# Kernel tuning notes

Measured on AMD Instinct MI355X. Metric: run time of the kernel, lower is better.

Reference implementation:

```python
import jax, jax.numpy as jnp
import numpy as np

B, C, H, W, K = 32, 10, 256, 256, 500
EPS = 1e-7


def setup_inputs() -> dict:
    key = jax.random.key(0)
    k1, k2, k3 = jax.random.split(key, 3)
    pred_wh = jax.random.normal(k1, (B, C, H, W), dtype=jnp.float32)
    wh_target = jax.random.normal(k2, (B, K, C), dtype=jnp.float32)
    reg_mask = jnp.ones((B, K), dtype=jnp.float32)
    ind = jax.random.randint(k3, (B, K), 0, H * W, dtype=jnp.int32)
    return {"pred_wh": pred_wh, "wh_target": wh_target, "reg_mask": reg_mask, "ind": ind}


def _cal_box(p):
    # p: [8] = (tt, rr, bb, ll) point offsets -> 4 corners centered at (tt+bb)/2
    tt, rr, bb, ll = p[0:2], p[2:4], p[4:6], p[6:8]
    cen = (tt + bb) * 0.5
    return jnp.stack([tt + rr, bb + rr, bb + ll, tt + ll]) - cen  # [4,2] tr,br,bl,tl


def _sort_ccw(pts):
    c = pts.mean(axis=0)
    ang = jnp.arctan2(pts[:, 1] - c[1], pts[:, 0] - c[0])
    return pts[jnp.argsort(ang)]


def _shoelace(pts):
    x, y = pts[:, 0], pts[:, 1]
    return 0.5 * jnp.abs(jnp.sum(x * jnp.roll(y, -1) - jnp.roll(x, -1) * y))


def _convex_inter_area(A, Bp):
    # A, Bp: [4,2] CCW-ordered convex quads. Intersection area via
    # candidate points (verts-inside + edge-edge crossings) of the convex overlap.
    An, Bn = jnp.roll(A, -1, axis=0), jnp.roll(Bp, -1, axis=0)

    def inside(P, poly, polyn):  # all-edges left-of test for CCW poly
        ex, ey = (polyn - poly)[:, 0], (polyn - poly)[:, 1]
        px = P[:, None, 0] - poly[None, :, 0]
        py = P[:, None, 1] - poly[None, :, 1]
        return jnp.all(ex[None, :] * py - ey[None, :] * px >= -EPS, axis=1)

    mA = inside(A, Bp, Bn)
    mB = inside(Bp, A, An)

    a1, a2 = A[:, None, :], An[:, None, :]
    b1, b2 = Bp[None, :, :], Bn[None, :, :]
    d1, d2 = a2 - a1, b2 - b1
    den = d1[..., 0] * d2[..., 1] - d1[..., 1] * d2[..., 0]
    diff = b1 - a1
    safe = jnp.where(jnp.abs(den) > EPS, den, 1.0)
    t = (diff[..., 0] * d2[..., 1] - diff[..., 1] * d2[..., 0]) / safe
    u = (diff[..., 0] * d1[..., 1] - diff[..., 1] * d1[..., 0]) / safe
    mI = (jnp.abs(den) > EPS) & (t >= -EPS) & (t <= 1 + EPS) & (u >= -EPS) & (u <= 1 + EPS)
    pI = a1 + t[..., None] * d1  # [4,4,2]

    pts = jnp.concatenate([A, Bp, pI.reshape(16, 2)], axis=0)  # [24,2]
    valid = jnp.concatenate([mA, mB, mI.reshape(16)], axis=0)  # [24]
    first = pts[jnp.argmax(valid)]
    pts = jnp.where(valid[:, None], pts, first)  # dup invalids onto a hull vertex
    nv = jnp.maximum(valid.sum(), 1)
    c = jnp.sum(pts * valid[:, None], axis=0) / nv
    ang = jnp.arctan2(pts[:, 1] - c[1], pts[:, 0] - c[0])
    area = _shoelace(pts[jnp.argsort(ang)])
    return jnp.where(valid.any(), area, 0.0)


def _per_box(a, b):
    A = _sort_ccw(_cal_box(a))
    Bq = _sort_ccw(_cal_box(b))
    inter = _convex_inter_area(A, Bq)
    union = _shoelace(A) + _shoelace(Bq) - inter
    iou = jnp.where(union > 0, inter / jnp.where(union > 0, union, 1.0), 0.0)

    w = jnp.sqrt((a[2] - a[6]) ** 2 + (a[3] - a[7]) ** 2)
    h = jnp.sqrt((a[0] - a[4]) ** 2 + (a[1] - a[5]) ** 2)
    wt = jnp.sqrt((b[2] - b[6]) ** 2 + (b[3] - a[7]) ** 2)  # faithful: source uses a[7]
    ht = jnp.sqrt((b[0] - b[4]) ** 2 + (b[1] - b[5]) ** 2)
    th1 = (a[3] - a[7]) / (a[2] - a[6])
    tth1 = (b[3] - b[7]) / (b[2] - b[6])
    th = (a[1] - a[5]) / (a[0] - a[4])
    tth = (b[1] - b[5]) / (b[0] - b[4])
    n = jnp.minimum((jnp.arctan(th) - jnp.arctan(tth)) ** 2,
                    (jnp.arctan(th1) - jnp.arctan(tth1)) ** 2)
    c4 = 4.0 / (np.pi ** 2)
    v = c4 * (jnp.arctan(wt / ht) - jnp.arctan(w / h)) ** 2
    s = c4 * n
    alpha = (v + s) / (1.0 - iou + v + s)
    return alpha * (v + 0.7 * s)


def reference(pred_wh, wh_target, reg_mask, ind):
    b, c, h, w = pred_wh.shape
    feat = pred_wh.transpose(0, 2, 3, 1).reshape(b, h * w, c)
    pred = jnp.take_along_axis(feat, ind[:, :, None].astype(jnp.int32), axis=1)  # [B,K,C]
    pa = pred.reshape(-1, c)[:, :8]
    ga = wh_target.reshape(-1, c)[:, :8]
    losses = jax.vmap(_per_box)(pa, ga)  # [B*K]
    mflat = reg_mask.reshape(-1) > 0
    n = mflat.shape[0]
    last = jnp.max(jnp.where(mflat, jnp.arange(n), -1))
    # original loop overwrites `loss` each iter -> final value is the LAST masked box
    loss = jnp.where(mflat.any(), losses[jnp.maximum(last, 0)], 0.0)
    # everything feeding the loss is under torch.no_grad()/numpy -> detached
    return jax.lax.stop_gradient(loss)
```

## Files before the change

kernel.cpp:

```cpp
#include <hip/hip_runtime.h>
#include <math.h>

#define BB 32
#define CC 10
#define HH 256
#define WW 256
#define KK 500

constexpr double DEPS = 1e-7;

__device__ inline double dshfl(double v, int lane) { return __shfl(v, lane, 64); }

__device__ inline double shoelace4(const double* x, const double* y) {
    double s = x[0]*y[1] - x[1]*y[0];
    s += x[1]*y[2] - x[2]*y[1];
    s += x[2]*y[3] - x[3]*y[2];
    s += x[3]*y[0] - x[0]*y[3];
    return 0.5 * fabs(s);
}

__device__ void cal_box_sorted(const double p[8], double X[4], double Y[4]) {
    double cenx = (p[0] + p[4]) * 0.5;
    double ceny = (p[1] + p[5]) * 0.5;
    double px[4] = { p[0] + p[2] - cenx, p[4] + p[2] - cenx,
                     p[4] + p[6] - cenx, p[0] + p[6] - cenx };
    double py[4] = { p[1] + p[3] - ceny, p[5] + p[3] - ceny,
                     p[5] + p[7] - ceny, p[1] + p[7] - ceny };
    double cx = (px[0] + px[1] + px[2] + px[3]) * 0.25;
    double cy = (py[0] + py[1] + py[2] + py[3]) * 0.25;
    float ang[4];
    #pragma unroll
    for (int i = 0; i < 4; ++i)
        ang[i] = atan2f((float)(py[i] - cy), (float)(px[i] - cx));
    int idx[4] = {0, 1, 2, 3};
    #pragma unroll
    for (int i = 1; i < 4; ++i) {
        int key = idx[i]; float ka = ang[key]; int j = i - 1;
        while (j >= 0 && ang[idx[j]] > ka) { idx[j + 1] = idx[j]; --j; }
        idx[j + 1] = key;
    }
    #pragma unroll
    for (int i = 0; i < 4; ++i) { X[i] = px[idx[i]]; Y[i] = py[idx[i]]; }
}

__global__ __launch_bounds__(1024)
void IouLoss_26766236189166_kernel(const float* __restrict__ pred_wh,
                                   const float* __restrict__ wh_target,
                                   const float* __restrict__ reg_mask,
                                   const int* __restrict__ ind,
                                   float* __restrict__ out) {
    __shared__ int s_wave[16];
    __shared__ int s_last;
    const int tid = threadIdx.x;

    const float4* rm = (const float4*)reg_mask;
    const int N4 = (BB * KK) / 4;
    int last = -1;
    for (int chunk = 3; chunk >= 0; --chunk) {
        int lmax = -1;
        int i = chunk * 1024 + tid;
        if (i < N4) {
            float4 v = rm[i];
            if (v.x > 0.f) lmax = 4 * i;
            if (v.y > 0.f) lmax = 4 * i + 1;
            if (v.z > 0.f) lmax = 4 * i + 2;
            if (v.w > 0.f) lmax = 4 * i + 3;
        }
        #pragma unroll
        for (int off = 32; off > 0; off >>= 1)
            lmax = max(lmax, __shfl_down(lmax, off, 64));
        if ((tid & 63) == 0) s_wave[tid >> 6] = lmax;
        __syncthreads();
        if (tid == 0) {
            int m = -1;
            #pragma unroll
            for (int w = 0; w < 16; ++w) m = max(m, s_wave[w]);
            s_last = m;
        }
        __syncthreads();
        last = s_last;
        if (last >= 0) break;
    }

    if (tid >= 64) return;
    const int k = tid;

    float loss = 0.0f;
    if (last >= 0) {
        const int b   = last / KK;
        const int kk_ = last - b * KK;
        const int pix = ind[last];

        double a[8], g[8];
        const float* pw = pred_wh + (size_t)b * CC * (HH * WW) + pix;
        const float* gt = wh_target + ((size_t)b * KK + kk_) * CC;
        #pragma unroll
        for (int c = 0; c < 8; ++c) a[c] = (double)pw[(size_t)c * (HH * WW)];
        #pragma unroll
        for (int c = 0; c < 8; ++c) g[c] = (double)gt[c];

        double AX[4], AY[4], BX[4], BY[4];
        cal_box_sorted(a, AX, AY);
        cal_box_sorted(g, BX, BY);

        bool valid = false; double px = 0.0, py = 0.0;
        if (k < 4) {
            bool ok = true;
            #pragma unroll
            for (int j = 0; j < 4; ++j) {
                int jn = (j + 1) & 3;
                double ex = BX[jn] - BX[j], ey = BY[jn] - BY[j];
                double qx = AX[k] - BX[j], qy = AY[k] - BY[j];
                ok = ok && (ex * qy - ey * qx >= -DEPS);
            }
            valid = ok; px = AX[k]; py = AY[k];
        } else if (k < 8) {
            int i = k - 4;
            bool ok = true;
            #pragma unroll
            for (int j = 0; j < 4; ++j) {
                int jn = (j + 1) & 3;
                double ex = AX[jn] - AX[j], ey = AY[jn] - AY[j];
                double qx = BX[i] - AX[j], qy = BY[i] - AY[j];
                ok = ok && (ex * qy - ey * qx >= -DEPS);
            }
            valid = ok; px = BX[i]; py = BY[i];
        } else if (k < 24) {
            int i = (k - 8) >> 2, j = (k - 8) & 3;
            int in_ = (i + 1) & 3, jn = (j + 1) & 3;
            double a1x = AX[i], a1y = AY[i];
            double d1x = AX[in_] - a1x, d1y = AY[in_] - a1y;
            double b1x = BX[j], b1y = BY[j];
            double d2x = BX[jn] - b1x, d2y = BY[jn] - b1y;
            double den = d1x * d2y - d1y * d2x;
            double dx = b1x - a1x, dy = b1y - a1y;
            bool dok = fabs(den) > DEPS;
            double safe = dok ? den : 1.0;
            double t = (dx * d2y - dy * d2x) / safe;
            double u = (dx * d1y - dy * d1x) / safe;
            valid = dok && (t >= -DEPS) && (t <= 1.0 + DEPS)
                        && (u >= -DEPS) && (u <= 1.0 + DEPS);
            px = a1x + t * d1x;
            py = a1y + t * d1y;
        }

        unsigned long long mv = __ballot(valid);
        bool any = (mv != 0ull);
        int nv  = __popcll(mv);
        int nvd = nv < 1 ? 1 : nv;
        int fi  = any ? ((int)__ffsll(mv) - 1) : 0;
        double fx = dshfl(px, fi), fy = dshfl(py, fi);
        if (k < 24 && !valid) { px = fx; py = fy; }

        double cxs = valid ? px : 0.0, cys = valid ? py : 0.0;
        #pragma unroll
        for (int off = 32; off > 0; off >>= 1) {
            cxs += __shfl_xor(cxs, off, 64);
            cys += __shfl_xor(cys, off, 64);
        }
        double cx = cxs / (double)nvd, cy = cys / (double)nvd;

        float ang = (k < 24) ? atan2f((float)(py - cy), (float)(px - cx)) : INFINITY;
        int r = 0;
        #pragma unroll
        for (int j = 0; j < 24; ++j) {
            float aj = __shfl(ang, j, 64);
            r += (aj < ang) || (aj == ang && j < k);
        }
        if (k >= 24) r = k;

        int addr = r << 2;
        int xlo = __builtin_amdgcn_ds_permute(addr, __double2loint(px));
        int xhi = __builtin_amdgcn_ds_permute(addr, __double2hiint(px));
        int ylo = __builtin_amdgcn_ds_permute(addr, __double2loint(py));
        int yhi = __builtin_amdgcn_ds_permute(addr, __double2hiint(py));
        double sxp = __hiloint2double(xhi, xlo);
        double syp = __hiloint2double(yhi, ylo);

        int nxt = (k < 23) ? (k + 1) : ((k == 23) ? 0 : k);
        double nx = dshfl(sxp, nxt);
        double ny = dshfl(syp, nxt);
        double term = (k < 24) ? (sxp * ny - nx * syp) : 0.0;
        #pragma unroll
        for (int off = 32; off > 0; off >>= 1)
            term += __shfl_xor(term, off, 64);
        double inter = any ? 0.5 * fabs(term) : 0.0;

        double areaA = shoelace4(AX, AY);
        double areaB = shoelace4(BX, BY);
        double uni = areaA + areaB - inter;
        double iou = (uni > 0.0) ? (inter / uni) : 0.0;

        double w  = sqrt((a[2]-a[6])*(a[2]-a[6]) + (a[3]-a[7])*(a[3]-a[7]));
        double h  = sqrt((a[0]-a[4])*(a[0]-a[4]) + (a[1]-a[5])*(a[1]-a[5]));
        double wt = sqrt((g[2]-g[6])*(g[2]-g[6]) + (g[3]-a[7])*(g[3]-a[7]));
        double ht = sqrt((g[0]-g[4])*(g[0]-g[4]) + (g[1]-g[5])*(g[1]-g[5]));

        double num = (k==0) ? (a[1]-a[5]) : (k==1) ? (g[1]-g[5]) :
                     (k==2) ? (a[3]-a[7]) : (k==3) ? (g[3]-g[7]) :
                     (k==4) ? wt : w;
        double den = (k==0) ? (a[0]-a[4]) : (k==1) ? (g[0]-g[4]) :
                     (k==2) ? (a[2]-a[6]) : (k==3) ? (g[2]-g[6]) :
                     (k==4) ? ht : h;
        double at = atan(num / den);
        double t_th   = dshfl(at, 0);
        double t_tth  = dshfl(at, 1);
        double t_th1  = dshfl(at, 2);
        double t_tth1 = dshfl(at, 3);
        double t_awt  = dshfl(at, 4);
        double t_aw   = dshfl(at, 5);

        double d1v = t_th  - t_tth;
        double d2v = t_th1 - t_tth1;
        double nn = fmin(d1v * d1v, d2v * d2v);
        const double c4 = 4.0 / (M_PI * M_PI);
        double dvv = t_awt - t_aw;
        double v = c4 * dvv * dvv;
        double sv = c4 * nn;
        double alpha = (v + sv) / (1.0 - iou + v + sv);
        loss = (float)(alpha * (v + 0.7 * sv));
    }

    if (tid == 0) out[0] = loss;
}

extern "C" void kernel_launch(void* const* d_in, const int* in_sizes, int n_in,
                              void* d_out, int out_size, void* d_ws, size_t ws_size,
                              hipStream_t stream) {
    const float* pred_wh   = (const float*)d_in[0];
    const float* wh_target = (const float*)d_in[1];
    const float* reg_mask  = (const float*)d_in[2];
    const int*   ind       = (const int*)d_in[3];
    float* out = (float*)d_out;
    IouLoss_26766236189166_kernel<<<dim3(1), dim3(1024), 0, stream>>>(
        pred_wh, wh_target, reg_mask, ind, out);
}
```

Measured before the change: 13.31 us.

## Scan reg_mask backward with a single wave and fuse ind lookup

```diff
diff --git a/kernel.cpp b/kernel.cpp
--- a/kernel.cpp
+++ b/kernel.cpp
@@ -43,53 +43,47 @@
     for (int i = 0; i < 4; ++i) { X[i] = px[idx[i]]; Y[i] = py[idx[i]]; }
 }
 
-__global__ __launch_bounds__(1024)
+__global__ __launch_bounds__(64)
 void IouLoss_26766236189166_kernel(const float* __restrict__ pred_wh,
                                    const float* __restrict__ wh_target,
                                    const float* __restrict__ reg_mask,
                                    const int* __restrict__ ind,
                                    float* __restrict__ out) {
-    __shared__ int s_wave[16];
-    __shared__ int s_last;
-    const int tid = threadIdx.x;
-
+    const int k = threadIdx.x;
     const float4* rm = (const float4*)reg_mask;
+    const int4*   iv = (const int4*)ind;
     const int N4 = (BB * KK) / 4;
-    int last = -1;
-    for (int chunk = 3; chunk >= 0; --chunk) {
-        int lmax = -1;
-        int i = chunk * 1024 + tid;
-        if (i < N4) {
+
+    int last = -1, pix = 0;
+    for (int base = N4 - 64; base > -64; base -= 64) {
+        int i = base + k;
+        int lmax = -1, pcand = 0;
+        if (i >= 0) {
             float4 v = rm[i];
-            if (v.x > 0.f) lmax = 4 * i;
-            if (v.y > 0.f) lmax = 4 * i + 1;
-            if (v.z > 0.f) lmax = 4 * i + 2;
-            if (v.w > 0.f) lmax = 4 * i + 3;
-        }
-        #pragma unroll
-        for (int off = 32; off > 0; off >>= 1)
-            lmax = max(lmax, __shfl_down(lmax, off, 64));
-        if ((tid & 63) == 0) s_wave[tid >> 6] = lmax;
-        __syncthreads();
-        if (tid == 0) {
-            int m = -1;
-            #pragma unroll
-            for (int w = 0; w < 16; ++w) m = max(m, s_wave[w]);
-            s_last = m;
-        }
-        __syncthreads();
-        last = s_last;
-        if (last >= 0) break;
+            int4  iq = iv[i];
+            if (v.x > 0.f) { lmax = 4*i;     pcand = iq.x; }
+            if (v.y > 0.f) { lmax = 4*i + 1; pcand = iq.y; }
+            if (v.z > 0.f) { lmax = 4*i + 2; pcand = iq.z; }
+            if (v.w > 0.f) { lmax = 4*i + 3; pcand = iq.w; }
+        }
+        unsigned long long packed =
+            ((unsigned long long)(unsigned)(lmax + 1) << 32) | (unsigned)pcand;
+        #pragma unroll
+        for (int off = 32; off > 0; off >>= 1) {
+            unsigned long long o = __shfl_xor(packed, off, 64);
+            packed = (o > packed) ? o : packed;
+        }
+        if ((packed >> 32) != 0ull) {
+            last = (int)(packed >> 32) - 1;
+            pix  = (int)(packed & 0xffffffffull);
+            break;
+        }
     }
-
-    if (tid >= 64) return;
-    const int k = tid;
 
     float loss = 0.0f;
     if (last >= 0) {
         const int b   = last / KK;
         const int kk_ = last - b * KK;
-        const int pix = ind[last];
 
         double a[8], g[8];
         const float* pw = pred_wh + (size_t)b * CC * (HH * WW) + pix;
@@ -221,7 +215,7 @@
         loss = (float)(alpha * (v + 0.7 * sv));
     }
 
-    if (tid == 0) out[0] = loss;
+    if (k == 0) out[0] = loss;
 }
 
 extern "C" void kernel_launch(void* const* d_in, const int* in_sizes, int n_in,
@@ -232,6 +226,6 @@
     const float* reg_mask  = (const float*)d_in[2];
     const int*   ind       = (const int*)d_in[3];
     float* out = (float*)d_out;
-    IouLoss_26766236189166_kernel<<<dim3(1), dim3(1024), 0, stream>>>(
+    IouLoss_26766236189166_kernel<<<dim3(1), dim3(64), 0, stream>>>(
         pred_wh, wh_target, reg_mask, ind, out);
 }
```

Result: faster. 12.58 us (-5.5%).
